# Optimization experiments

Measured on AMD Instinct MI355X. Metric: run time of the kernel, lower is better.

Reference implementation:

```python
import jax, jax.numpy as jnp
import numpy as np

# ---- static irreps config: 128x0e + 128x1e + 128x2e (in == out) ----
MULS = (128, 128, 128)
LS = (0, 1, 2)
DIM = sum(m * (2 * l + 1) for m, l in zip(MULS, LS))  # 1152
N_EDGES = 32768


def _m_indices(m):
    # column indices selected by m_in_mask[m] / m_out_mask[m], in ascending order
    idx, off = [], 0
    for mul, l in zip(MULS, LS):
        k = 2 * l + 1
        if l >= m:
            for j in range(mul):
                base = off + j * k
                if m == 0:
                    idx.append(base + l)
                else:
                    idx.extend([base + l - m, base + l + m])
        off += mul * k
    return np.asarray(idx, dtype=np.int32)

IDX = [_m_indices(m) for m in range(3)]

_S3 = float(np.sqrt(3.0) / 2.0)
J_MATS = {
    1: np.array([[0.0, 1, 0], [1, 0, 0], [0, 0, -1]], np.float32),
    2: np.array([[0.0, 0, 0, -1, 0],
                 [0, 1, 0, 0, 0],
                 [0, 0, -0.5, 0, -_S3],
                 [-1, 0, 0, 0, 0],
                 [0, 0, -_S3, 0, 0.5]], np.float32),
}


def _z_rot(a, l):
    # matches torch _z_rot: diag cos(f*a) + anti-diag (flipped) sin(f*a), f = l..-l
    freqs = jnp.arange(l, -l - 1, -1, dtype=a.dtype)
    d = jnp.cos(freqs * a[:, None])   # (n, 2l+1)
    ad = jnp.sin(freqs * a[:, None])
    eye = jnp.eye(2 * l + 1, dtype=a.dtype)
    return d[..., None] * eye + jnp.flip(ad[..., None] * eye, axis=-1)


def _wigner(l, alpha, beta):
    Jl = jnp.asarray(J_MATS[l], dtype=alpha.dtype)
    return _z_rot(alpha, l) @ Jl @ _z_rot(beta, l) @ Jl  # gamma = 0 -> Z(0)=I


def setup_inputs() -> dict:
    key = jax.random.key(0)
    ks = jax.random.split(key, 6)
    x = jax.random.normal(ks[0], (N_EDGES, DIM), jnp.float32)
    R = jax.random.normal(ks[1], (N_EDGES, 3), jnp.float32)
    W0 = jax.random.normal(ks[2], (384, 384), jnp.float32) / np.sqrt(384.0)
    b0 = 0.01 * jax.random.normal(ks[3], (384,), jnp.float32)
    W1 = jax.random.normal(ks[4], (512, 256), jnp.float32) / np.sqrt(2.0 * 256.0)
    W2 = jax.random.normal(ks[5], (256, 128), jnp.float32) / np.sqrt(2.0 * 128.0)
    return {"x": x, "R": R, "W0": W0, "b0": b0, "W1": W1, "W2": W2}


def _forward(x, R, W0, b0, W1, W2):
    n = x.shape[0]
    # xyz_to_angles(R[:, [1, 2, 0]])
    v = jnp.take(R, jnp.array([1, 2, 0]), axis=1)
    v = v / jnp.clip(jnp.linalg.norm(v, axis=1, keepdims=True), 1e-12)
    beta = jnp.arccos(jnp.clip(v[:, 1], -1.0, 1.0))
    alpha = jnp.arctan2(v[:, 0], v[:, 2])
    D1 = _wigner(1, alpha, beta)  # (n,3,3)
    D2 = _wigner(2, alpha, beta)  # (n,5,5)

    # rotate input irreps (l > 0) into edge-aligned frame: D^T x per l-block
    b1 = x[:, 128:512].reshape(n, 128, 3)
    b2 = x[:, 512:1152].reshape(n, 128, 5)
    r1 = jnp.einsum('nji,nmj->nmi', D1, b1).reshape(n, -1)
    r2 = jnp.einsum('nji,nmj->nmi', D2, b2).reshape(n, -1)
    x_rot = jnp.concatenate([x[:, :128], r1, r2], axis=1)

    out = jnp.zeros((n, DIM), dtype=x.dtype)

    # m = 0 path: gather m=0 components, zero out l=0 scalar inputs, fc0
    seg0 = x_rot[:, IDX[0]]  # (n, 384)
    seg0 = jnp.concatenate([jnp.zeros_like(seg0[:, :128]), seg0[:, 128:]], axis=1)
    out = out.at[:, IDX[0]].add(seg0 @ W0.T + b0)

    # m >= 1 paths: gather, complex-style small GEMM, scatter back
    for m, W in ((1, W1), (2, W2)):
        seg = x_rot[:, IDX[m]].reshape(n, 2, -1)          # (n, 2, num_in_m)
        y = jnp.einsum('ncj,kj->nck', seg, W)              # (n, 2, 2*num_out_m)
        no = y.shape[-1] // 2
        out_re = y[:, 0, :no] - y[:, 1, no:]
        out_im = y[:, 0, no:] + y[:, 1, :no]
        out = out.at[:, IDX[m]].add(jnp.concatenate([out_re, out_im], axis=1))

    # rotate output irreps (l > 0) back to the original frame: D y per l-block
    o1 = jnp.einsum('nij,nmj->nmi', D1, out[:, 128:512].reshape(n, 128, 3)).reshape(n, -1)
    o2 = jnp.einsum('nij,nmj->nmi', D2, out[:, 512:1152].reshape(n, 128, 5)).reshape(n, -1)
    return jnp.concatenate([out[:, :128], o1, o2], axis=1)


def reference(x, R, W0, b0, W1, W2):
    return _forward(x, R, W0, b0, W1, W2)
```

## Files before the change

kernel.cpp:

```cpp
#include <hip/hip_runtime.h>
#include <cstddef>
#include <cstdint>


typedef _Float16 f16x8 __attribute__((ext_vector_type(8)));
typedef _Float16 f16x2 __attribute__((ext_vector_type(2)));
typedef float    f32x4 __attribute__((ext_vector_type(4)));

#define AS1 __attribute__((address_space(1)))
#define AS3 __attribute__((address_space(3)))

__device__ __forceinline__ void mm3(const float* A, const float* B, float* C) {
#pragma unroll
  for (int i = 0; i < 3; ++i)
#pragma unroll
    for (int j = 0; j < 3; ++j)
      C[i*3+j] = fmaf(A[i*3+0], B[0*3+j], fmaf(A[i*3+1], B[1*3+j], A[i*3+2]*B[2*3+j]));
}

__device__ __forceinline__ void mm5(const float* A, const float* B, float* C) {
#pragma unroll
  for (int i = 0; i < 5; ++i)
#pragma unroll
    for (int j = 0; j < 5; ++j) {
      float s = 0.f;
#pragma unroll
      for (int k = 0; k < 5; ++k) s = fmaf(A[i*5+k], B[k*5+j], s);
      C[i*5+j] = s;
    }
}

__global__ __launch_bounds__(256) void wigner_k(const float* __restrict__ R,
                                                float* __restrict__ D1buf,
                                                float* __restrict__ D2buf, int n) {
  int e = blockIdx.x*256 + threadIdx.x;
  if (e >= n) return;
  float r0 = R[3*e+0], r1 = R[3*e+1], r2 = R[3*e+2];
  float v0 = r1, v1 = r2, v2 = r0;
  float nrm = fmaxf(sqrtf(v0*v0 + v1*v1 + v2*v2), 1e-12f);
  float inv = 1.0f/nrm;
  v0 *= inv; v1 *= inv; v2 *= inv;

  float cb = fminf(fmaxf(v1, -1.f), 1.f);
  float sb = sqrtf(fmaxf(1.f - cb*cb, 0.f));
  float h = sqrtf(v0*v0 + v2*v2);
  float ca, sa;
  if (h > 1e-20f) { float ih = 1.f/h; ca = v2*ih; sa = v0*ih; }
  else            { ca = 1.f; sa = 0.f; }

  {
    float Za[9] = {ca,0,sa, 0,1,0, -sa,0,ca};
    float Zb[9] = {cb,0,sb, 0,1,0, -sb,0,cb};
    const float J1[9] = {0,1,0, 1,0,0, 0,0,-1};
    float T[9], T2[9], D1[9];
    mm3(Zb, J1, T); mm3(J1, T, T2); mm3(Za, T2, D1);
#pragma unroll
    for (int i = 0; i < 9; ++i) D1buf[(size_t)e*9 + i] = D1[i];
  }
  {
    float c2a = ca*ca - sa*sa, s2a = 2.f*ca*sa;
    float c2b = cb*cb - sb*sb, s2b = 2.f*cb*sb;
    float Za2[25] = {
      c2a, 0,   0, 0,   s2a,
      0,   ca,  0, sa,  0,
      0,   0,   1, 0,   0,
      0,  -sa,  0, ca,  0,
     -s2a, 0,   0, 0,   c2a};
    float Zb2[25] = {
      c2b, 0,   0, 0,   s2b,
      0,   cb,  0, sb,  0,
      0,   0,   1, 0,   0,
      0,  -sb,  0, cb,  0,
     -s2b, 0,   0, 0,   c2b};
    const float S3 = 0.8660254037844386f;
    const float J2[25] = {
      0, 0, 0,    -1, 0,
      0, 1, 0,     0, 0,
      0, 0, -0.5f, 0, -S3,
     -1, 0, 0,     0, 0,
      0, 0, -S3,   0, 0.5f};
    float T[25], T2[25], D2[25];
    mm5(Zb2, J2, T); mm5(J2, T, T2); mm5(Za2, T2, D2);
#pragma unroll
    for (int i = 0; i < 25; ++i) D2buf[(size_t)e*25 + i] = D2[i];
  }
}

__global__ __launch_bounds__(256) void build_mats(const float* __restrict__ W0,
                                                  const float* __restrict__ b0,
                                                  const float* __restrict__ W1,
                                                  const float* __restrict__ W2,
                                                  _Float16* __restrict__ M0,
                                                  float* __restrict__ B0,
                                                  _Float16* __restrict__ M1,
                                                  _Float16* __restrict__ M2) {
  int i = blockIdx.x*256 + threadIdx.x;
  if (i < 98304) {
    int k = i >> 8, j = i & 255;
    M0[i] = (_Float16)W0[k*384 + 128 + j];
  } else if (i < 98688) {
    B0[i - 98304] = b0[i - 98304];
  } else if (i < 360832) {
    int idx = i - 98688;
    int k = idx >> 9, j = idx & 511;
    float val;
    if (k < 256) val = (j < 256) ? W1[k*256 + j] : -W1[(k+256)*256 + (j-256)];
    else         val = (j < 256) ? W1[k*256 + j] :  W1[(k-256)*256 + (j-256)];
    M1[idx] = (_Float16)val;
  } else if (i < 426368) {
    int idx = i - 360832;
    int k = idx >> 8, j = idx & 255;
    float val;
    if (k < 128) val = (j < 128) ? W2[k*128 + j] : -W2[(k+128)*128 + (j-128)];
    else         val = (j < 128) ? W2[k*128 + j] :  W2[(k-128)*128 + (j-128)];
    M2[idx] = (_Float16)val;
  }
}

__global__ __launch_bounds__(256) void rotate_gather(const float* __restrict__ x,
                                                     const float* __restrict__ D1buf,
                                                     const float* __restrict__ D2buf,
                                                     _Float16* __restrict__ U, int n) {
  const int tid = blockIdx.x*256 + threadIdx.x;
  const int e = tid >> 7;
  const int c = tid & 127;
  if (e >= n) return;

  float d1[9], d2[25];
#pragma unroll
  for (int i = 0; i < 9; ++i) d1[i] = D1buf[(size_t)e*9 + i];
#pragma unroll
  for (int i = 0; i < 25; ++i) d2[i] = D2buf[(size_t)e*25 + i];

  const float* xr = x + (size_t)e*1152;
  _Float16* Ur = U + (size_t)e*1024;

  float b0 = xr[128 + 3*c + 0];
  float b1 = xr[128 + 3*c + 1];
  float b2 = xr[128 + 3*c + 2];
  float r0 = fmaf(d1[0], b0, fmaf(d1[3], b1, d1[6]*b2));
  float r1 = fmaf(d1[1], b0, fmaf(d1[4], b1, d1[7]*b2));
  float r2 = fmaf(d1[2], b0, fmaf(d1[5], b1, d1[8]*b2));
  Ur[c] = (_Float16)r1;
  { f16x2 t; t[0] = (_Float16)r0; t[1] = (_Float16)r2;
    *(f16x2*)&Ur[256 + 2*c] = t; }

  float q0 = xr[512 + 5*c + 0];
  float q1 = xr[512 + 5*c + 1];
  float q2 = xr[512 + 5*c + 2];
  float q3 = xr[512 + 5*c + 3];
  float q4 = xr[512 + 5*c + 4];
  float rr[5];
#pragma unroll
  for (int i = 0; i < 5; ++i)
    rr[i] = fmaf(d2[0*5+i], q0, fmaf(d2[1*5+i], q1, fmaf(d2[2*5+i], q2,
             fmaf(d2[3*5+i], q3, d2[4*5+i]*q4))));
  Ur[128 + c] = (_Float16)rr[2];
  { f16x2 t; t[0] = (_Float16)rr[1]; t[1] = (_Float16)rr[3];
    *(f16x2*)&Ur[512 + 2*c] = t; }
  { f16x2 t; t[0] = (_Float16)rr[0]; t[1] = (_Float16)rr[4];
    if (c < 64) *(f16x2*)&Ur[768 + 2*c] = t;
    else        *(f16x2*)&Ur[896 + 2*(c-64)] = t; }
}

__global__ __launch_bounds__(256) void gemm_mfma(const _Float16* __restrict__ U,
                                                 const _Float16* __restrict__ M0,
                                                 const float* __restrict__ B0,
                                                 const _Float16* __restrict__ M1,
                                                 const _Float16* __restrict__ M2,
                                                 _Float16* __restrict__ C, int n) {
  const int bid = blockIdx.x;
  const int x8 = bid & 7;
  const int g  = bid >> 3;
  const int rr = g / 9;
  const int sec = g - rr*9;
  const int rowBase = (rr*8 + x8) * 128;

  int K, Aoff, Coff, colTile;
  const _Float16* Mp;
  const float* bias = nullptr;
  if (sec < 3)      { K = 256; Aoff = 0;   Coff = 0;   colTile = sec;     Mp = M0; bias = B0; }
  else if (sec < 7) { K = 512; Aoff = 256; Coff = 384; colTile = sec - 3; Mp = M1; }
  else              { K = 256; Aoff = 768; Coff = 896; colTile = sec - 7; Mp = M2; }
  const int colBase = colTile * 128;

  __shared__ __align__(16) _Float16 Als[128*64];
  __shared__ __align__(16) _Float16 Bls[128*64];

  const int t  = threadIdx.x;
  const int w  = t >> 6, l = t & 63;
  const int wr = w >> 1, wc = w & 1;
  const int fr = l & 15, g0 = l >> 4;

  const char* Ag = (const char*)(U + (size_t)rowBase*1024 + Aoff);
  const char* Bg = (const char*)(Mp + (size_t)colBase*K);
  const int sprime = (l & 7) ^ (l >> 3);
  const int rl = l >> 3;

  f32x4 acc[4][4];
#pragma unroll
  for (int m = 0; m < 4; ++m)
#pragma unroll
    for (int nn = 0; nn < 4; ++nn) { f32x4 z = {0.f,0.f,0.f,0.f}; acc[m][nn] = z; }

  for (int kk = 0; kk < K; kk += 64) {
#pragma unroll
    for (int cc = 0; cc < 4; ++cc) {
      const int c = w + cc*4;
      const int r = c*8 + rl;
      __builtin_amdgcn_global_load_lds(
          (const AS1 void*)(Ag + (size_t)r*2048 + (size_t)kk*2 + sprime*16),
          (AS3 void*)((char*)Als + c*1024), 16, 0, 0);
      __builtin_amdgcn_global_load_lds(
          (const AS1 void*)(Bg + (size_t)r*(size_t)(K*2) + (size_t)kk*2 + sprime*16),
          (AS3 void*)((char*)Bls + c*1024), 16, 0, 0);
    }
    __syncthreads();

#pragma unroll
    for (int h = 0; h < 2; ++h) {
      const int sidx = h*4 + g0;
      f16x8 af[4], bf[4];
#pragma unroll
      for (int m = 0; m < 4; ++m) {
        const int row = wr*64 + m*16 + fr;
        af[m] = *(const f16x8*)((const char*)Als + row*128 + ((sidx ^ (row & 7))*16));
      }
#pragma unroll
      for (int nn = 0; nn < 4; ++nn) {
        const int col = wc*64 + nn*16 + fr;
        bf[nn] = *(const f16x8*)((const char*)Bls + col*128 + ((sidx ^ (col & 7))*16));
      }
#pragma unroll
      for (int m = 0; m < 4; ++m)
#pragma unroll
        for (int nn = 0; nn < 4; ++nn)
          acc[m][nn] = __builtin_amdgcn_mfma_f32_16x16x32_f16(af[m], bf[nn], acc[m][nn], 0, 0, 0);
    }
    __syncthreads();
  }

  float bv[4];
#pragma unroll
  for (int nn = 0; nn < 4; ++nn)
    bv[nn] = bias ? bias[colBase + wc*64 + nn*16 + fr] : 0.f;
#pragma unroll
  for (int m = 0; m < 4; ++m) {
    const int row0 = rowBase + wr*64 + m*16 + g0*4;
#pragma unroll
    for (int nn = 0; nn < 4; ++nn) {
      const int vc = Coff + colBase + wc*64 + nn*16 + fr;
#pragma unroll
      for (int j = 0; j < 4; ++j)
        C[(size_t)(row0 + j)*1152 + vc] = (_Float16)(acc[m][nn][j] + bv[nn]);
    }
  }
}

__global__ __launch_bounds__(256) void rotate_back2(const _Float16* __restrict__ V,
                                                    float* __restrict__ out,
                                                    const float* __restrict__ D1buf,
                                                    const float* __restrict__ D2buf, int n) {
  const int tid = blockIdx.x*256 + threadIdx.x;
  const int e = tid >> 7;
  const int c = tid & 127;
  if (e >= n) return;

  float d1[9], d2[25];
#pragma unroll
  for (int i = 0; i < 9; ++i) d1[i] = D1buf[(size_t)e*9 + i];
#pragma unroll
  for (int i = 0; i < 25; ++i) d2[i] = D2buf[(size_t)e*25 + i];

  const _Float16* Vr = V + (size_t)e*1152;
  float* orow = out + (size_t)e*1152;

  orow[c] = (float)Vr[c];

  f16x2 pp = *(const f16x2*)&Vr[384 + 2*c];
  float p0 = (float)pp[0], p2 = (float)pp[1];
  float p1 = (float)Vr[128 + c];
  orow[128 + 3*c + 0] = fmaf(d1[0], p0, fmaf(d1[1], p1, d1[2]*p2));
  orow[128 + 3*c + 1] = fmaf(d1[3], p0, fmaf(d1[4], p1, d1[5]*p2));
  orow[128 + 3*c + 2] = fmaf(d1[6], p0, fmaf(d1[7], p1, d1[8]*p2));

  f16x2 qq = (c < 64) ? *(const f16x2*)&Vr[896 + 2*c]
                      : *(const f16x2*)&Vr[1024 + 2*(c-64)];
  float q0 = (float)qq[0], q4 = (float)qq[1];
  f16x2 q13 = *(const f16x2*)&Vr[640 + 2*c];
  float q1 = (float)q13[0], q3 = (float)q13[1];
  float q2 = (float)Vr[256 + c];
#pragma unroll
  for (int i = 0; i < 5; ++i)
    orow[512 + 5*c + i] = fmaf(d2[i*5+0], q0, fmaf(d2[i*5+1], q1, fmaf(d2[i*5+2], q2,
                           fmaf(d2[i*5+3], q3, d2[i*5+4]*q4))));
}

extern "C" void kernel_launch(void* const* d_in, const int* in_sizes, int n_in,
                              void* d_out, int out_size, void* d_ws, size_t ws_size,
                              hipStream_t stream) {
  const float* x  = (const float*)d_in[0];
  const float* R  = (const float*)d_in[1];
  const float* W0 = (const float*)d_in[2];
  const float* b0 = (const float*)d_in[3];
  const float* W1 = (const float*)d_in[4];
  const float* W2 = (const float*)d_in[5];
  float* out = (float*)d_out;

  const int n = in_sizes[0] / 1152;

  char* p = (char*)d_ws;
  _Float16* V16 = (_Float16*)p;  p += (size_t)n*1152*2;
  _Float16* U16 = (_Float16*)p;  p += (size_t)n*1024*2;
  float* D1buf  = (float*)p;     p += (size_t)n*9*4;
  float* D2buf  = (float*)p;     p += (size_t)n*25*4;
  _Float16* M0h = (_Float16*)p;  p += 196608;
  _Float16* M1h = (_Float16*)p;  p += 524288;
  _Float16* M2h = (_Float16*)p;  p += 131072;
  float* B0f    = (float*)p;

  wigner_k<<<(n + 255)/256, 256, 0, stream>>>(R, D1buf, D2buf, n);
  build_mats<<<(426368 + 255)/256, 256, 0, stream>>>(W0, b0, W1, W2, M0h, B0f, M1h, M2h);
  rotate_gather<<<n/2, 256, 0, stream>>>(x, D1buf, D2buf, U16, n);
  gemm_mfma<<<(n/128)*9, 256, 0, stream>>>(U16, M0h, B0f, M1h, M2h, V16, n);
  rotate_back2<<<n/2, 256, 0, stream>>>(V16, out, D1buf, D2buf, n);
}
```

Before: 346.3 us.

## Fuse rotate-gather into GEMM with whole-row U tile in LDS

Merges the rotate_gather kernel into the MFMA GEMM. Each 512-thread block now rotates 64 edges into a swizzled 128KB LDS tile and then loops over all nine output column tiles, streaming only the weight tiles from global memory. This drops the fp16 U intermediate's global write and re-read. In exchange it uses a large LDS footprint (about 144KB per block) that limits occupancy, switches to smaller 64x128 tiles with fewer MFMAs per wave, and serialises the gather phase before any GEMM work in a block.

Result: slower. 367.0 us (+6.0%).

```diff
diff --git a/kernel.cpp b/kernel.cpp
--- a/kernel.cpp
+++ b/kernel.cpp
@@ -117,142 +117,140 @@
   }
 }
 
-__global__ __launch_bounds__(256) void rotate_gather(const float* __restrict__ x,
-                                                     const float* __restrict__ D1buf,
-                                                     const float* __restrict__ D2buf,
-                                                     _Float16* __restrict__ U, int n) {
-  const int tid = blockIdx.x*256 + threadIdx.x;
-  const int e = tid >> 7;
-  const int c = tid & 127;
-  if (e >= n) return;
-
-  float d1[9], d2[25];
-#pragma unroll
-  for (int i = 0; i < 9; ++i) d1[i] = D1buf[(size_t)e*9 + i];
-#pragma unroll
-  for (int i = 0; i < 25; ++i) d2[i] = D2buf[(size_t)e*25 + i];
-
-  const float* xr = x + (size_t)e*1152;
-  _Float16* Ur = U + (size_t)e*1024;
-
-  float b0 = xr[128 + 3*c + 0];
-  float b1 = xr[128 + 3*c + 1];
-  float b2 = xr[128 + 3*c + 2];
-  float r0 = fmaf(d1[0], b0, fmaf(d1[3], b1, d1[6]*b2));
-  float r1 = fmaf(d1[1], b0, fmaf(d1[4], b1, d1[7]*b2));
-  float r2 = fmaf(d1[2], b0, fmaf(d1[5], b1, d1[8]*b2));
-  Ur[c] = (_Float16)r1;
-  { f16x2 t; t[0] = (_Float16)r0; t[1] = (_Float16)r2;
-    *(f16x2*)&Ur[256 + 2*c] = t; }
-
-  float q0 = xr[512 + 5*c + 0];
-  float q1 = xr[512 + 5*c + 1];
-  float q2 = xr[512 + 5*c + 2];
-  float q3 = xr[512 + 5*c + 3];
-  float q4 = xr[512 + 5*c + 4];
-  float rr[5];
-#pragma unroll
-  for (int i = 0; i < 5; ++i)
-    rr[i] = fmaf(d2[0*5+i], q0, fmaf(d2[1*5+i], q1, fmaf(d2[2*5+i], q2,
-             fmaf(d2[3*5+i], q3, d2[4*5+i]*q4))));
-  Ur[128 + c] = (_Float16)rr[2];
-  { f16x2 t; t[0] = (_Float16)rr[1]; t[1] = (_Float16)rr[3];
-    *(f16x2*)&Ur[512 + 2*c] = t; }
-  { f16x2 t; t[0] = (_Float16)rr[0]; t[1] = (_Float16)rr[4];
-    if (c < 64) *(f16x2*)&Ur[768 + 2*c] = t;
-    else        *(f16x2*)&Ur[896 + 2*(c-64)] = t; }
-}
-
-__global__ __launch_bounds__(256) void gemm_mfma(const _Float16* __restrict__ U,
-                                                 const _Float16* __restrict__ M0,
-                                                 const float* __restrict__ B0,
-                                                 const _Float16* __restrict__ M1,
-                                                 const _Float16* __restrict__ M2,
-                                                 _Float16* __restrict__ C, int n) {
-  const int bid = blockIdx.x;
-  const int x8 = bid & 7;
-  const int g  = bid >> 3;
-  const int rr = g / 9;
-  const int sec = g - rr*9;
-  const int rowBase = (rr*8 + x8) * 128;
-
-  int K, Aoff, Coff, colTile;
-  const _Float16* Mp;
-  const float* bias = nullptr;
-  if (sec < 3)      { K = 256; Aoff = 0;   Coff = 0;   colTile = sec;     Mp = M0; bias = B0; }
-  else if (sec < 7) { K = 512; Aoff = 256; Coff = 384; colTile = sec - 3; Mp = M1; }
-  else              { K = 256; Aoff = 768; Coff = 896; colTile = sec - 7; Mp = M2; }
-  const int colBase = colTile * 128;
-
-  __shared__ __align__(16) _Float16 Als[128*64];
+__global__ __launch_bounds__(512) void rg_gemm(const float* __restrict__ x,
+                                               const float* __restrict__ D1buf,
+                                               const float* __restrict__ D2buf,
+                                               const _Float16* __restrict__ M0,
+                                               const float* __restrict__ B0,
+                                               const _Float16* __restrict__ M1,
+                                               const _Float16* __restrict__ M2,
+                                               _Float16* __restrict__ C, int n) {
+  __shared__ __align__(16) _Float16 Uls[64*1024];
   __shared__ __align__(16) _Float16 Bls[128*64];
 
-  const int t  = threadIdx.x;
-  const int w  = t >> 6, l = t & 63;
-  const int wr = w >> 1, wc = w & 1;
+  const int t = threadIdx.x;
+  const int rowBase = blockIdx.x * 64;
+
+  {
+    const int elo = t >> 7;
+    const int c   = t & 127;
+#pragma unroll 1
+    for (int it = 0; it < 16; ++it) {
+      const int el = it*4 + elo;
+      const int e  = rowBase + el;
+      float d1[9], d2[25];
+#pragma unroll
+      for (int i = 0; i < 9; ++i)  d1[i] = D1buf[(size_t)e*9 + i];
+#pragma unroll
+      for (int i = 0; i < 25; ++i) d2[i] = D2buf[(size_t)e*25 + i];
+      const float* xr = x + (size_t)e*1152;
+
+      float b0 = xr[128 + 3*c + 0];
+      float b1 = xr[128 + 3*c + 1];
+      float b2 = xr[128 + 3*c + 2];
+      float r0 = fmaf(d1[0], b0, fmaf(d1[3], b1, d1[6]*b2));
+      float r1 = fmaf(d1[1], b0, fmaf(d1[4], b1, d1[7]*b2));
+      float r2 = fmaf(d1[2], b0, fmaf(d1[5], b1, d1[8]*b2));
+      float q0 = xr[512 + 5*c + 0];
+      float q1 = xr[512 + 5*c + 1];
+      float q2 = xr[512 + 5*c + 2];
+      float q3 = xr[512 + 5*c + 3];
+      float q4 = xr[512 + 5*c + 4];
+      float rr[5];
+#pragma unroll
+      for (int i = 0; i < 5; ++i)
+        rr[i] = fmaf(d2[0*5+i], q0, fmaf(d2[1*5+i], q1, fmaf(d2[2*5+i], q2,
+                 fmaf(d2[3*5+i], q3, d2[4*5+i]*q4))));
+
+      char* Ub = (char*)Uls + el*2048;
+      const int ex = (el & 7);
+      auto put = [&](int v, float val) {
+        *(_Float16*)(Ub + ((((v>>3) ^ ex)<<4) | ((v&7)<<1))) = (_Float16)val;
+      };
+      put(c, r1);
+      put(256 + 2*c, r0);
+      put(257 + 2*c, r2);
+      put(128 + c, rr[2]);
+      put(512 + 2*c, rr[1]);
+      put(513 + 2*c, rr[3]);
+      if (c < 64) { put(768 + 2*c, rr[0]);        put(769 + 2*c, rr[4]); }
+      else        { put(896 + 2*(c-64), rr[0]);   put(897 + 2*(c-64), rr[4]); }
+    }
+  }
+  __syncthreads();
+
+  const int w = t >> 6, l = t & 63;
+  const int wr = w >> 2, wc = w & 3;
   const int fr = l & 15, g0 = l >> 4;
-
-  const char* Ag = (const char*)(U + (size_t)rowBase*1024 + Aoff);
-  const char* Bg = (const char*)(Mp + (size_t)colBase*K);
   const int sprime = (l & 7) ^ (l >> 3);
   const int rl = l >> 3;
 
-  f32x4 acc[4][4];
-#pragma unroll
-  for (int m = 0; m < 4; ++m)
-#pragma unroll
-    for (int nn = 0; nn < 4; ++nn) { f32x4 z = {0.f,0.f,0.f,0.f}; acc[m][nn] = z; }
-
-  for (int kk = 0; kk < K; kk += 64) {
-#pragma unroll
-    for (int cc = 0; cc < 4; ++cc) {
-      const int c = w + cc*4;
-      const int r = c*8 + rl;
-      __builtin_amdgcn_global_load_lds(
-          (const AS1 void*)(Ag + (size_t)r*2048 + (size_t)kk*2 + sprime*16),
-          (AS3 void*)((char*)Als + c*1024), 16, 0, 0);
-      __builtin_amdgcn_global_load_lds(
-          (const AS1 void*)(Bg + (size_t)r*(size_t)(K*2) + (size_t)kk*2 + sprime*16),
-          (AS3 void*)((char*)Bls + c*1024), 16, 0, 0);
+#pragma unroll 1
+  for (int j = 0; j < 9; ++j) {
+    int K, Aoff, Coff, colBase;
+    const _Float16* Mp;
+    const float* bias = nullptr;
+    if (j < 3)      { K = 256; Aoff = 0;   Coff = 0;   colBase = j*128;     Mp = M0; bias = B0; }
+    else if (j < 7) { K = 512; Aoff = 256; Coff = 384; colBase = (j-3)*128; Mp = M1; }
+    else            { K = 256; Aoff = 768; Coff = 896; colBase = (j-7)*128; Mp = M2; }
+
+    const char* Bg = (const char*)(Mp + (size_t)colBase*K);
+
+    f32x4 acc[2][2];
+#pragma unroll
+    for (int m = 0; m < 2; ++m)
+#pragma unroll
+      for (int nn = 0; nn < 2; ++nn) { f32x4 z = {0.f,0.f,0.f,0.f}; acc[m][nn] = z; }
+
+    for (int kk = 0; kk < K; kk += 64) {
+#pragma unroll
+      for (int cc = 0; cc < 2; ++cc) {
+        const int ch = w*2 + cc;
+        const int r = ch*8 + rl;
+        __builtin_amdgcn_global_load_lds(
+            (const AS1 void*)(Bg + (size_t)r*(size_t)(K*2) + (size_t)kk*2 + sprime*16),
+            (AS3 void*)((char*)Bls + ch*1024), 16, 0, 0);
+      }
+      __syncthreads();
+
+#pragma unroll
+      for (int h = 0; h < 2; ++h) {
+        const int sidx = h*4 + g0;
+        const int gseg = ((Aoff + kk) >> 3) + sidx;
+        f16x8 af[2], bf[2];
+#pragma unroll
+        for (int m = 0; m < 2; ++m) {
+          const int row = wr*32 + m*16 + fr;
+          af[m] = *(const f16x8*)((const char*)Uls + row*2048 + ((gseg ^ (row & 7))<<4));
+        }
+#pragma unroll
+        for (int nn = 0; nn < 2; ++nn) {
+          const int col = wc*32 + nn*16 + fr;
+          bf[nn] = *(const f16x8*)((const char*)Bls + col*128 + ((sidx ^ (col & 7))*16));
+        }
+#pragma unroll
+        for (int m = 0; m < 2; ++m)
+#pragma unroll
+          for (int nn = 0; nn < 2; ++nn)
+            acc[m][nn] = __builtin_amdgcn_mfma_f32_16x16x32_f16(af[m], bf[nn], acc[m][nn], 0, 0, 0);
+      }
+      __syncthreads();
     }
-    __syncthreads();
-
-#pragma unroll
-    for (int h = 0; h < 2; ++h) {
-      const int sidx = h*4 + g0;
-      f16x8 af[4], bf[4];
-#pragma unroll
-      for (int m = 0; m < 4; ++m) {
-        const int row = wr*64 + m*16 + fr;
-        af[m] = *(const f16x8*)((const char*)Als + row*128 + ((sidx ^ (row & 7))*16));
+
+    float bv[2];
+#pragma unroll
+    for (int nn = 0; nn < 2; ++nn)
+      bv[nn] = bias ? bias[colBase + wc*32 + nn*16 + fr] : 0.f;
+#pragma unroll
+    for (int m = 0; m < 2; ++m) {
+      const int row0 = rowBase + wr*32 + m*16 + g0*4;
+#pragma unroll
+      for (int nn = 0; nn < 2; ++nn) {
+        const int vc = Coff + colBase + wc*32 + nn*16 + fr;
+#pragma unroll
+        for (int jj = 0; jj < 4; ++jj)
+          C[(size_t)(row0 + jj)*1152 + vc] = (_Float16)(acc[m][nn][jj] + bv[nn]);
       }
-#pragma unroll
-      for (int nn = 0; nn < 4; ++nn) {
-        const int col = wc*64 + nn*16 + fr;
-        bf[nn] = *(const f16x8*)((const char*)Bls + col*128 + ((sidx ^ (col & 7))*16));
-      }
-#pragma unroll
-      for (int m = 0; m < 4; ++m)
-#pragma unroll
-        for (int nn = 0; nn < 4; ++nn)
-          acc[m][nn] = __builtin_amdgcn_mfma_f32_16x16x32_f16(af[m], bf[nn], acc[m][nn], 0, 0, 0);
-    }
-    __syncthreads();
-  }
-
-  float bv[4];
-#pragma unroll
-  for (int nn = 0; nn < 4; ++nn)
-    bv[nn] = bias ? bias[colBase + wc*64 + nn*16 + fr] : 0.f;
-#pragma unroll
-  for (int m = 0; m < 4; ++m) {
-    const int row0 = rowBase + wr*64 + m*16 + g0*4;
-#pragma unroll
-    for (int nn = 0; nn < 4; ++nn) {
-      const int vc = Coff + colBase + wc*64 + nn*16 + fr;
-#pragma unroll
-      for (int j = 0; j < 4; ++j)
-        C[(size_t)(row0 + j)*1152 + vc] = (_Float16)(acc[m][nn][j] + bv[nn]);
     }
   }
 }
@@ -311,7 +309,6 @@
 
   char* p = (char*)d_ws;
   _Float16* V16 = (_Float16*)p;  p += (size_t)n*1152*2;
-  _Float16* U16 = (_Float16*)p;  p += (size_t)n*1024*2;
   float* D1buf  = (float*)p;     p += (size_t)n*9*4;
   float* D2buf  = (float*)p;     p += (size_t)n*25*4;
   _Float16* M0h = (_Float16*)p;  p += 196608;
@@ -321,7 +318,6 @@
 
   wigner_k<<<(n + 255)/256, 256, 0, stream>>>(R, D1buf, D2buf, n);
   build_mats<<<(426368 + 255)/256, 256, 0, stream>>>(W0, b0, W1, W2, M0h, B0f, M1h, M2h);
-  rotate_gather<<<n/2, 256, 0, stream>>>(x, D1buf, D2buf, U16, n);
-  gemm_mfma<<<(n/128)*9, 256, 0, stream>>>(U16, M0h, B0f, M1h, M2h, V16, n);
+  rg_gemm<<<n/64, 512, 0, stream>>>(x, D1buf, D2buf, M0h, B0f, M1h, M2h, V16, n);
   rotate_back2<<<n/2, 256, 0, stream>>>(V16, out, D1buf, D2buf, n);
 }
```
